# Kernel tuning notes

Hardware: AMD Instinct MI355X
Metric: run time of the kernel (lower is better)

## Reference

```python
import jax, jax.numpy as jnp
import numpy as np

D_K = 1024
D_V = 1024
D_IN = 1024
D_MODEL = 1024
NUM_HEADS = 16


def setup_inputs() -> dict:
    key = jax.random.key(0)
    k1, k2, k3, k4, k5 = jax.random.split(key, 5)
    x = jax.random.normal(k1, (4, 2048, D_IN), dtype=jnp.float32)
    # trunc_normal init approximated by clipped normal
    W_Q = jnp.clip(jax.random.normal(k2, (D_K, D_IN), dtype=jnp.float32), -2.0, 2.0)
    W_K = jnp.clip(jax.random.normal(k3, (D_K, D_IN), dtype=jnp.float32), -2.0, 2.0)
    W_V = jnp.clip(jax.random.normal(k4, (D_V, D_IN), dtype=jnp.float32), -2.0, 2.0)
    W_O = jnp.clip(jax.random.normal(k5, (D_MODEL, D_V), dtype=jnp.float32), -2.0, 2.0)
    return {"x": x, "W_Q": W_Q, "W_K": W_K, "W_V": W_V, "W_O": W_O}


def reference(x, W_Q, W_K, W_V, W_O):
    b, s, _ = x.shape
    h = NUM_HEADS
    hd_k = D_K // h
    hd_v = D_V // h
    wq = W_Q.reshape(h, hd_k, D_IN)
    wk = W_K.reshape(h, hd_k, D_IN)
    wv = W_V.reshape(h, hd_v, D_IN)
    # project: [b, h, s, head_dim]
    q = jnp.einsum('hkd,bsd->bhsk', wq, x)
    k = jnp.einsum('hkd,bsd->bhsk', wk, x)
    v = jnp.einsum('hvd,bsd->bhsv', wv, x)
    scale = 1.0 / jnp.sqrt(jnp.float32(hd_k))
    scores = jnp.einsum('bhnk,bhmk->bhnm', q, k) * scale  # [b,h,s,s]
    causal = jnp.tril(jnp.ones((s, s), dtype=bool))
    scores = jnp.where(causal, scores, -jnp.inf)
    attn = jax.nn.softmax(scores, axis=-1)
    out = jnp.einsum('bhnm,bhmv->bhnv', attn, v)  # [b,h,s,hd_v]
    out = out.transpose(0, 2, 1, 3).reshape(b, s, D_V)  # concat heads
    return jnp.einsum('ov,bsv->bso', W_O, out)
```

## Files before the change

### kernel.cpp

```cpp
#include <hip/hip_runtime.h>
#include <hip/hip_bf16.h>

typedef __bf16 bf16_t;
typedef __bf16 bf16x4 __attribute__((ext_vector_type(4)));
typedef __bf16 bf16x8 __attribute__((ext_vector_type(8)));
typedef float f32x4 __attribute__((ext_vector_type(4)));

#define MFMA16(a, b, c) __builtin_amdgcn_mfma_f32_16x16x32_bf16((a), (b), (c), 0, 0, 0)

#if __has_builtin(__builtin_amdgcn_exp2f)
#define EXP2(x) __builtin_amdgcn_exp2f(x)
#else
#define EXP2(x) exp2f(x)
#endif

__device__ inline void g2l16(const void* g, void* l) {
    __builtin_amdgcn_global_load_lds((const __attribute__((address_space(1))) void*)g,
                                     (__attribute__((address_space(3))) void*)l, 16, 0, 0);
}

__global__ __launch_bounds__(256) void cvt_split_k(const float* __restrict__ src,
                                                   bf16_t* __restrict__ hi,
                                                   bf16_t* __restrict__ lo, int n4) {
    int i = blockIdx.x * 256 + threadIdx.x;
    if (i < n4) {
        float4 v = reinterpret_cast<const float4*>(src)[i];
        bf16x4 h, l;
        float f;
        f = v.x; h[0] = (__bf16)f; l[0] = (__bf16)(f - (float)h[0]);
        f = v.y; h[1] = (__bf16)f; l[1] = (__bf16)(f - (float)h[1]);
        f = v.z; h[2] = (__bf16)f; l[2] = (__bf16)(f - (float)h[2]);
        f = v.w; h[3] = (__bf16)f; l[3] = (__bf16)(f - (float)h[3]);
        reinterpret_cast<bf16x4*>(hi)[i] = h;
        reinterpret_cast<bf16x4*>(lo)[i] = l;
    }
}

__global__ __launch_bounds__(256) void cvt_weights_k(const float* __restrict__ Wq,
                                                     const float* __restrict__ Wk,
                                                     const float* __restrict__ Wv,
                                                     const float* __restrict__ Wo,
                                                     bf16_t* __restrict__ WQKh, bf16_t* __restrict__ WQKl,
                                                     bf16_t* __restrict__ Wvh, bf16_t* __restrict__ Woh) {
    const int i = blockIdx.x * 256 + threadIdx.x;
    const int which = blockIdx.y;
    if (which <= 1) {
        const float c = (which == 0) ? 0.125f * 1.4426950408889634f : 1.0f;
        const int off = which * 262144;
        float4 v = reinterpret_cast<const float4*>(which == 0 ? Wq : Wk)[i];
        bf16x4 h, l;
        float f;
        f = v.x * c; h[0] = (__bf16)f; l[0] = (__bf16)(f - (float)h[0]);
        f = v.y * c; h[1] = (__bf16)f; l[1] = (__bf16)(f - (float)h[1]);
        f = v.z * c; h[2] = (__bf16)f; l[2] = (__bf16)(f - (float)h[2]);
        f = v.w * c; h[3] = (__bf16)f; l[3] = (__bf16)(f - (float)h[3]);
        reinterpret_cast<bf16x4*>(WQKh)[i + off] = h;
        reinterpret_cast<bf16x4*>(WQKl)[i + off] = l;
    } else {
        float4 v = reinterpret_cast<const float4*>(which == 2 ? Wv : Wo)[i];
        bf16x4 o;
        o[0] = (__bf16)v.x; o[1] = (__bf16)v.y; o[2] = (__bf16)v.z; o[3] = (__bf16)v.w;
        reinterpret_cast<bf16x4*>(which == 2 ? Wvh : Woh)[i] = o;
    }
}

template <int LGX>
__device__ inline void xcd_tile(int& bm, int& bn) {
    const int id = blockIdx.y * (1 << LGX) + blockIdx.x;
    const int cpx = ((1 << LGX) * gridDim.y) >> 3;
    const int swz = (id & 7) * cpx + (id >> 3);
    bn = swz & ((1 << LGX) - 1);
    bm = swz >> LGX;
}

template <int MODE>
__global__ __launch_bounds__(256) void gemm_bt(const bf16_t* __restrict__ A,
                                               const bf16_t* __restrict__ B,
                                               void* __restrict__ Cout,
                                               int M, int N, int K) {
    __shared__ __align__(16) bf16_t As[128 * 32];
    __shared__ __align__(16) bf16_t Bs[128 * 32];
    const int tid = threadIdx.x;
    const int w = tid >> 6, lane = tid & 63;
    const int l15 = lane & 15, g = lane >> 4;
    const int wr = w >> 1, wc = w & 1;
    int bm, bn;
    xcd_tile<3>(bm, bn);

    const f32x4 fz = {0.f, 0.f, 0.f, 0.f};
    f32x4 acc[4][4];
#pragma unroll
    for (int m = 0; m < 4; m++)
#pragma unroll
        for (int n = 0; n < 4; n++) acc[m][n] = fz;

    const bf16_t* Ab = A + (size_t)bm * 128 * K;
    const bf16_t* Bb = B + (size_t)bn * 128 * K;
    const int rowL = w * 16 + (lane >> 2);
    const int c8 = (lane & 3) * 8;
    char* AsD = (char*)As + w * 1024;
    char* BsD = (char*)Bs + w * 1024;

    for (int k0 = 0; k0 < K; k0 += 32) {
        g2l16(Ab + (size_t)rowL * K + k0 + c8, AsD);
        g2l16(Ab + (size_t)(rowL + 64) * K + k0 + c8, AsD + 4096);
        g2l16(Bb + (size_t)rowL * K + k0 + c8, BsD);
        g2l16(Bb + (size_t)(rowL + 64) * K + k0 + c8, BsD + 4096);
        __syncthreads();

        bf16x8 af[4], bfr[4];
        const bf16x8* Ap = reinterpret_cast<const bf16x8*>(As + (wr * 64 + l15) * 32 + g * 8);
#pragma unroll
        for (int m = 0; m < 4; m++) af[m] = Ap[m * 64];
        const bf16x8* Bp = reinterpret_cast<const bf16x8*>(Bs + (wc * 64 + l15) * 32 + g * 8);
#pragma unroll
        for (int n = 0; n < 4; n++) bfr[n] = Bp[n * 64];
#pragma unroll
        for (int m = 0; m < 4; m++)
#pragma unroll
            for (int n = 0; n < 4; n++) acc[m][n] = MFMA16(af[m], bfr[n], acc[m][n]);
        __syncthreads();
    }

    const int row0 = bm * 128 + wr * 64 + g * 4;
    const int col0 = bn * 128 + wc * 64 + l15;
#pragma unroll
    for (int m = 0; m < 4; m++)
#pragma unroll
        for (int n = 0; n < 4; n++)
#pragma unroll
            for (int r = 0; r < 4; r++) {
                int row = row0 + m * 16 + r;
                int col = col0 + n * 16;
                float v = acc[m][n][r];
                if (MODE == 0) {
                    ((bf16_t*)Cout)[(size_t)row * N + col] = (__bf16)v;
                } else if (MODE == 1) {
                    int b = row >> 11, s = row & 2047;
                    ((bf16_t*)Cout)[((size_t)b * N + col) * 2048 + s] = (__bf16)v;
                } else {
                    ((float*)Cout)[(size_t)row * N + col] = v;
                }
            }
}

__global__ __launch_bounds__(256) void gemm_splitQK(const bf16_t* __restrict__ Ah,
                                                    const bf16_t* __restrict__ Al,
                                                    const bf16_t* __restrict__ Bh,
                                                    const bf16_t* __restrict__ Bl,
                                                    bf16_t* __restrict__ Qh,
                                                    bf16_t* __restrict__ Ql,
                                                    bf16_t* __restrict__ Kh,
                                                    bf16_t* __restrict__ Kl,
                                                    int K) {
    __shared__ __align__(16) bf16_t Ash[128 * 32];
    __shared__ __align__(16) bf16_t Asl[128 * 32];
    __shared__ __align__(16) bf16_t Bsh[128 * 32];
    __shared__ __align__(16) bf16_t Bsl[128 * 32];
    const int tid = threadIdx.x;
    const int w = tid >> 6, lane = tid & 63;
    const int l15 = lane & 15, g = lane >> 4;
    const int wr = w >> 1, wc = w & 1;
    int bm, bn;
    xcd_tile<4>(bm, bn);

    const f32x4 fz = {0.f, 0.f, 0.f, 0.f};
    f32x4 acc[4][4];
#pragma unroll
    for (int m = 0; m < 4; m++)
#pragma unroll
        for (int n = 0; n < 4; n++) acc[m][n] = fz;

    const size_t aoff = (size_t)bm * 128 * K;
    const size_t boff = (size_t)bn * 128 * K;
    const int rowL = w * 16 + (lane >> 2);
    const int c8 = (lane & 3) * 8;
    const size_t g0 = (size_t)rowL * K + c8;
    const size_t g1 = (size_t)(rowL + 64) * K + c8;

    for (int k0 = 0; k0 < K; k0 += 32) {
        g2l16(Ah + aoff + g0 + k0, (char*)Ash + w * 1024);
        g2l16(Ah + aoff + g1 + k0, (char*)Ash + w * 1024 + 4096);
        g2l16(Al + aoff + g0 + k0, (char*)Asl + w * 1024);
        g2l16(Al + aoff + g1 + k0, (char*)Asl + w * 1024 + 4096);
        g2l16(Bh + boff + g0 + k0, (char*)Bsh + w * 1024);
        g2l16(Bh + boff + g1 + k0, (char*)Bsh + w * 1024 + 4096);
        g2l16(Bl + boff + g0 + k0, (char*)Bsl + w * 1024);
        g2l16(Bl + boff + g1 + k0, (char*)Bsl + w * 1024 + 4096);
        __syncthreads();

        bf16x8 ah[4], al[4], bh[4], bl[4];
        const int ao = (wr * 64 + l15) * 32 + g * 8;
        const int bo = (wc * 64 + l15) * 32 + g * 8;
#pragma unroll
        for (int m = 0; m < 4; m++) {
            ah[m] = *reinterpret_cast<const bf16x8*>(Ash + ao + m * 512);
            al[m] = *reinterpret_cast<const bf16x8*>(Asl + ao + m * 512);
        }
#pragma unroll
        for (int n = 0; n < 4; n++) {
            bh[n] = *reinterpret_cast<const bf16x8*>(Bsh + bo + n * 512);
            bl[n] = *reinterpret_cast<const bf16x8*>(Bsl + bo + n * 512);
        }
#pragma unroll
        for (int m = 0; m < 4; m++)
#pragma unroll
            for (int n = 0; n < 4; n++) {
                acc[m][n] = MFMA16(ah[m], bh[n], acc[m][n]);
                acc[m][n] = MFMA16(al[m], bh[n], acc[m][n]);
                acc[m][n] = MFMA16(ah[m], bl[n], acc[m][n]);
            }
        __syncthreads();
    }

    bf16_t* Ch = (bn < 8) ? Qh : Kh;
    bf16_t* Cl = (bn < 8) ? Ql : Kl;
    const int row0 = bm * 128 + wr * 64 + g * 4;
    const int col0 = (bn * 128 + wc * 64 + l15) & 1023;
#pragma unroll
    for (int m = 0; m < 4; m++)
#pragma unroll
        for (int n = 0; n < 4; n++)
#pragma unroll
            for (int r = 0; r < 4; r++) {
                size_t idx = (size_t)(row0 + m * 16 + r) * 1024 + col0 + n * 16;
                float v = acc[m][n][r];
                bf16_t h = (__bf16)v;
                Ch[idx] = h;
                Cl[idx] = (__bf16)(v - (float)h);
            }
}

__global__ __launch_bounds__(256) void attn_k(const bf16_t* __restrict__ Qh,
                                              const bf16_t* __restrict__ Ql,
                                              const bf16_t* __restrict__ Kh,
                                              const bf16_t* __restrict__ Kl,
                                              const bf16_t* __restrict__ Vt,
                                              bf16_t* __restrict__ Opart,
                                              float* __restrict__ ML) {
    const int px = blockIdx.x;
    const int h = blockIdx.y;
    const int b = blockIdx.z >> 1, hf = blockIdx.z & 1;
    const int tid = threadIdx.x, w = tid >> 6, lane = tid & 63;
    const int l15 = lane & 15, g = lane >> 4;

    __shared__ __align__(16) bf16_t Ks[4096];
    __shared__ __align__(16) bf16_t Ls[4096];
    __shared__ __align__(16) bf16_t Vs[4096];
    __shared__ __align__(16) bf16_t Ps[4][1024];

    const size_t boff = (size_t)b * 2048 * 1024;
    const size_t vbase = (size_t)b * 1024 * 2048 + (size_t)(h * 64) * 2048;

    const int sr = tid >> 3;
    const int sc = tid & 7;
    const int wo0 = sr * 8 + (sc ^ (sr & 7));
    const int wo1 = wo0 + 256;

    int4 sK0, sK1, sL0, sL1, sV0, sV1;
#define STAGE_LOAD(T)                                                               \
    do {                                                                            \
        const int kv0_ = (T) * 64;                                                  \
        const bf16_t* kp = Kh + boff + (size_t)(kv0_ + sr) * 1024 + h * 64 + sc * 8;\
        const bf16_t* lp = Kl + boff + (size_t)(kv0_ + sr) * 1024 + h * 64 + sc * 8;\
        const bf16_t* vp = Vt + vbase + (size_t)sr * 2048 + kv0_ + sc * 8;          \
        sK0 = *(const int4*)kp; sK1 = *(const int4*)(kp + 32 * 1024);               \
        sL0 = *(const int4*)lp; sL1 = *(const int4*)(lp + 32 * 1024);               \
        sV0 = *(const int4*)vp; sV1 = *(const int4*)(vp + 32 * 2048);               \
    } while (0)
#define STAGE_WRITE()                                                               \
    do {                                                                            \
        ((int4*)Ks)[wo0] = sK0; ((int4*)Ks)[wo1] = sK1;                             \
        ((int4*)Ls)[wo0] = sL0; ((int4*)Ls)[wo1] = sL1;                             \
        ((int4*)Vs)[wo0] = sV0; ((int4*)Vs)[wo1] = sV1;                             \
    } while (0)

    const f32x4 fz = {0.f, 0.f, 0.f, 0.f};
    bf16_t* Op = Opart + (size_t)hf * 8 * 1024 * 1024;
    float* MLp = ML + (size_t)hf * 8192 * 16 * 2;

#pragma unroll 1
    for (int it = 0; it < 2; ++it) {
        const int qt = it ? (15 - px) : px;
        const int qrw = qt * 128 + w * 32;

        bf16x8 qhf[2][2], qlf[2][2];
#pragma unroll
        for (int m = 0; m < 2; m++)
#pragma unroll
            for (int kk = 0; kk < 2; kk++) {
                size_t qi = boff + (size_t)(qrw + m * 16 + l15) * 1024 + h * 64 + kk * 32 + g * 8;
                qhf[m][kk] = *reinterpret_cast<const bf16x8*>(Qh + qi);
                qlf[m][kk] = *reinterpret_cast<const bf16x8*>(Ql + qi);
            }

        f32x4 oacc[2][4];
#pragma unroll
        for (int m = 0; m < 2; m++)
#pragma unroll
            for (int n = 0; n < 4; n++) oacc[m][n] = fz;
        float mst[2] = {-__builtin_inff(), -__builtin_inff()};
        float lst[2] = {0.f, 0.f};

        const int t0 = hf ? qt + 1 : 0;
        const int t1 = hf ? 2 * qt + 1 : qt;
        STAGE_LOAD(t0);
        STAGE_WRITE();
        __syncthreads();

        for (int t = t0; t <= t1; ++t) {
            const int kv0 = t * 64;
            if (t < t1) STAGE_LOAD(t + 1);

            if (kv0 <= qrw + 31) {
                f32x4 st[2][4];
#pragma unroll
                for (int m = 0; m < 2; m++)
#pragma unroll
                    for (int n = 0; n < 4; n++) st[m][n] = fz;
                __builtin_amdgcn_s_setprio(1);
#pragma unroll
                for (int kk = 0; kk < 2; kk++)
#pragma unroll
                    for (int n = 0; n < 4; n++) {
                        const int off = (n * 16 + l15) * 64 + (((kk * 4 + g) ^ (l15 & 7)) << 3);
                        bf16x8 khf = *reinterpret_cast<const bf16x8*>(&Ks[off]);
                        bf16x8 klf = *reinterpret_cast<const bf16x8*>(&Ls[off]);
#pragma unroll
                        for (int m = 0; m < 2; m++) {
                            st[m][n] = MFMA16(khf, qhf[m][kk], st[m][n]);
                            st[m][n] = MFMA16(khf, qlf[m][kk], st[m][n]);
                            st[m][n] = MFMA16(klf, qhf[m][kk], st[m][n]);
                        }
                    }
                __builtin_amdgcn_s_setprio(0);

                const bool diag = (kv0 + 63 > qrw);
#pragma unroll
                for (int m = 0; m < 2; m++) {
                    const int qrow = qrw + m * 16 + l15;
                    float pmax = -__builtin_inff();
                    if (diag) {
                        const int klim = qrow - kv0;
#pragma unroll
                        for (int n = 0; n < 4; n++)
#pragma unroll
                            for (int r = 0; r < 4; r++) {
                                float s = st[m][n][r];
                                if (n * 16 + g * 4 + r > klim) s = -__builtin_inff();
                                st[m][n][r] = s;
                                pmax = fmaxf(pmax, s);
                            }
                    } else {
#pragma unroll
                        for (int n = 0; n < 4; n++)
#pragma unroll
                            for (int r = 0; r < 4; r++) pmax = fmaxf(pmax, st[m][n][r]);
                    }
                    pmax = fmaxf(pmax, __shfl_xor(pmax, 16));
                    pmax = fmaxf(pmax, __shfl_xor(pmax, 32));
                    const float mn = fmaxf(mst[m], pmax);
                    const float alpha = EXP2(mst[m] - mn);
                    mst[m] = mn;
                    float rs = 0.f;
#pragma unroll
                    for (int n = 0; n < 4; n++)
#pragma unroll
                        for (int r = 0; r < 4; r++) {
                            float pe = EXP2(st[m][n][r] - mn);
                            st[m][n][r] = pe;
                            rs += pe;
                        }
                    rs += __shfl_xor(rs, 16);
                    rs += __shfl_xor(rs, 32);
                    lst[m] = lst[m] * alpha + rs;
#pragma unroll
                    for (int n = 0; n < 4; n++) oacc[m][n] *= alpha;

#pragma unroll
                    for (int n = 0; n < 4; n++) {
                        bf16x4 p4;
#pragma unroll
                        for (int r = 0; r < 4; r++) p4[r] = (__bf16)st[m][n][r];
                        const int chunk = (2 * n + (g >> 1)) ^ (l15 & 7);
                        *reinterpret_cast<bf16x4*>(&Ps[w][l15 * 64 + chunk * 8 + (g & 1) * 4]) = p4;
                    }

                    asm volatile("s_waitcnt lgkmcnt(0)" ::: "memory");
                    __builtin_amdgcn_sched_barrier(0);

                    __builtin_amdgcn_s_setprio(1);
#pragma unroll
                    for (int kk = 0; kk < 2; kk++) {
                        bf16x8 pa = *reinterpret_cast<const bf16x8*>(
                            &Ps[w][l15 * 64 + (((kk * 4 + g) ^ (l15 & 7)) << 3)]);
#pragma unroll
                        for (int n = 0; n < 4; n++) {
                            const int voff = (n * 16 + l15) * 64 + (((kk * 4 + g) ^ (l15 & 7)) << 3);
                            bf16x8 vf = *reinterpret_cast<const bf16x8*>(&Vs[voff]);
                            oacc[m][n] = MFMA16(vf, pa, oacc[m][n]);
                        }
                    }
                    __builtin_amdgcn_s_setprio(0);
                }
            }
            __syncthreads();
            if (t < t1) STAGE_WRITE();
            __syncthreads();
        }

#pragma unroll
        for (int m = 0; m < 2; m++) {
            const int qrow = qrw + m * 16 + l15;
#pragma unroll
            for (int n = 0; n < 4; n++) {
                bf16x4 o4;
#pragma unroll
                for (int r = 0; r < 4; r++) o4[r] = (__bf16)oacc[m][n][r];
                *reinterpret_cast<bf16x4*>(&Op[boff + (size_t)qrow * 1024 + h * 64 + n * 16 + g * 4]) = o4;
            }
            if (g == 0) {
                const int grow = b * 2048 + qrow;
                MLp[(grow * 16 + h) * 2 + 0] = mst[m];
                MLp[(grow * 16 + h) * 2 + 1] = lst[m];
            }
        }
    }
#undef STAGE_LOAD
#undef STAGE_WRITE
}

__global__ __launch_bounds__(256) void attn_combine_k(const bf16_t* __restrict__ Op0,
                                                      const bf16_t* __restrict__ Op1,
                                                      const float* __restrict__ ML,
                                                      bf16_t* __restrict__ O) {
    const int t = blockIdx.x * 256 + threadIdx.x;
    const int row = t >> 7;
    const int h = (t >> 3) & 15;
    const float m1 = ML[(row * 16 + h) * 2 + 0];
    const float l1 = ML[(row * 16 + h) * 2 + 1];
    const float m2 = ML[(8192 * 16 + row * 16 + h) * 2 + 0];
    const float l2 = ML[(8192 * 16 + row * 16 + h) * 2 + 1];
    const float mx = fmaxf(m1, m2);
    float w1 = (l1 > 0.f) ? EXP2(m1 - mx) : 0.f;
    float w2 = (l2 > 0.f) ? EXP2(m2 - mx) : 0.f;
    const float inv = 1.f / (l1 * w1 + l2 * w2);
    w1 *= inv; w2 *= inv;
    bf16x8 a = reinterpret_cast<const bf16x8*>(Op0)[t];
    bf16x8 c = reinterpret_cast<const bf16x8*>(Op1)[t];
    bf16x8 o;
#pragma unroll
    for (int i = 0; i < 8; i++) o[i] = (__bf16)((float)a[i] * w1 + (float)c[i] * w2);
    reinterpret_cast<bf16x8*>(O)[t] = o;
}

extern "C" void kernel_launch(void* const* d_in, const int* in_sizes, int n_in,
                              void* d_out, int out_size, void* d_ws, size_t ws_size,
                              hipStream_t stream) {
    const float* x  = (const float*)d_in[0];
    const float* Wq = (const float*)d_in[1];
    const float* Wk = (const float*)d_in[2];
    const float* Wv = (const float*)d_in[3];
    const float* Wo = (const float*)d_in[4];

    char* ws = (char*)d_ws;
    const size_t MB = (size_t)1 << 20;
    bf16_t* xh   = (bf16_t*)(ws);
    bf16_t* xl   = (bf16_t*)(ws + 16 * MB);
    bf16_t* Qh   = (bf16_t*)(ws + 32 * MB);
    bf16_t* Ql   = (bf16_t*)(ws + 48 * MB);
    bf16_t* Kh   = (bf16_t*)(ws + 64 * MB);
    bf16_t* Kl   = (bf16_t*)(ws + 80 * MB);
    bf16_t* Vt   = (bf16_t*)(ws + 96 * MB);
    bf16_t* Ob   = (bf16_t*)(ws + 112 * MB);
    bf16_t* WQKh = (bf16_t*)(ws + 128 * MB);
    bf16_t* WQKl = (bf16_t*)(ws + 132 * MB);
    bf16_t* Wvh  = (bf16_t*)(ws + 136 * MB);
    bf16_t* Woh  = (bf16_t*)(ws + 138 * MB);
    bf16_t* Opart = (bf16_t*)(ws);
    float*  ML    = (float*)(ws + 128 * MB);

    cvt_split_k<<<8192, 256, 0, stream>>>(x, xh, xl, 2097152);
    cvt_weights_k<<<dim3(1024, 4), 256, 0, stream>>>(Wq, Wk, Wv, Wo,
                                                     WQKh, WQKl, Wvh, Woh);

    gemm_splitQK<<<dim3(16, 64), 256, 0, stream>>>(xh, xl, WQKh, WQKl,
                                                   Qh, Ql, Kh, Kl, 1024);
    gemm_bt<1><<<dim3(8, 64), 256, 0, stream>>>(xh, Wvh, Vt, 8192, 1024, 1024);

    attn_k<<<dim3(8, 16, 8), 256, 0, stream>>>(Qh, Ql, Kh, Kl, Vt, Opart, ML);
    attn_combine_k<<<4096, 256, 0, stream>>>(Opart, Opart + (size_t)8 * 1024 * 1024, ML, Ob);

    gemm_bt<2><<<dim3(8, 64), 256, 0, stream>>>(Ob, Woh, d_out, 8192, 1024, 1024);
}
```

Measured before the change: 296.5 us.

## Stage V-transpose epilogue in LDS, remap attention blocks, lazily rescale softmax

The MODE 1 GEMM epilogue now transposes the tile through a padded LDS buffer and writes V^T with 16-byte stores instead of scattered 2-byte strided stores. The attention kernel remaps its block index so that neighbouring blocks share heads, batches and K/V data, aiming for better cache locality. Online softmax now skips the running-max update and output rescale unless some lane's max grew by more than 8 (log2 units), which saves exps and multiplies. The lazy rescale lets probabilities run up to 2^8 before bf16 rounding, a small precision risk, and the extra LDS tile raises shared-memory use in the GEMM.

Result: slower. 355.7 us (+20.0%).

```diff
diff --git a/kernel.cpp b/kernel.cpp
--- a/kernel.cpp
+++ b/kernel.cpp
@@ -122,26 +122,52 @@
         __syncthreads();
     }
 
-    const int row0 = bm * 128 + wr * 64 + g * 4;
-    const int col0 = bn * 128 + wc * 64 + l15;
-#pragma unroll
-    for (int m = 0; m < 4; m++)
-#pragma unroll
-        for (int n = 0; n < 4; n++)
-#pragma unroll
-            for (int r = 0; r < 4; r++) {
-                int row = row0 + m * 16 + r;
-                int col = col0 + n * 16;
-                float v = acc[m][n][r];
-                if (MODE == 0) {
-                    ((bf16_t*)Cout)[(size_t)row * N + col] = (__bf16)v;
-                } else if (MODE == 1) {
-                    int b = row >> 11, s = row & 2047;
-                    ((bf16_t*)Cout)[((size_t)b * N + col) * 2048 + s] = (__bf16)v;
-                } else {
-                    ((float*)Cout)[(size_t)row * N + col] = v;
+    if constexpr (MODE == 1) {
+        __shared__ __align__(16) bf16_t Ct[128][130];
+        const int colL = wc * 64 + l15;
+        const int rowB = wr * 64 + g * 4;
+#pragma unroll
+        for (int m = 0; m < 4; m++)
+#pragma unroll
+            for (int n = 0; n < 4; n++) {
+                bf16x4 c4;
+#pragma unroll
+                for (int r = 0; r < 4; r++) c4[r] = (__bf16)acc[m][n][r];
+                *reinterpret_cast<bf16x4*>(&Ct[colL + n * 16][rowB + m * 16]) = c4;
+            }
+        __syncthreads();
+        const int bb = (bm * 128) >> 11;
+        const int s0 = (bm * 128) & 2047;
+        const int vg = tid >> 3, scc = tid & 7;
+        bf16_t* Vtb = (bf16_t*)Cout + (size_t)bb * 1024 * 2048;
+#pragma unroll
+        for (int u = 0; u < 4; u++)
+#pragma unroll
+            for (int hh = 0; hh < 2; hh++) {
+                const int v = u * 32 + vg;
+                const int s = hh * 64 + scc * 8;
+                *reinterpret_cast<int4*>(&Vtb[(size_t)(bn * 128 + v) * 2048 + s0 + s]) =
+                    *reinterpret_cast<const int4*>(&Ct[v][s]);
+            }
+    } else {
+        const int row0 = bm * 128 + wr * 64 + g * 4;
+        const int col0 = bn * 128 + wc * 64 + l15;
+#pragma unroll
+        for (int m = 0; m < 4; m++)
+#pragma unroll
+            for (int n = 0; n < 4; n++)
+#pragma unroll
+                for (int r = 0; r < 4; r++) {
+                    int row = row0 + m * 16 + r;
+                    int col = col0 + n * 16;
+                    float v = acc[m][n][r];
+                    if (MODE == 0) {
+                        ((bf16_t*)Cout)[(size_t)row * N + col] = (__bf16)v;
+                    } else {
+                        ((float*)Cout)[(size_t)row * N + col] = v;
+                    }
                 }
-            }
+    }
 }
 
 __global__ __launch_bounds__(256) void gemm_splitQK(const bf16_t* __restrict__ Ah,
@@ -238,9 +264,12 @@
                                               const bf16_t* __restrict__ Vt,
                                               bf16_t* __restrict__ Opart,
                                               float* __restrict__ ML) {
-    const int px = blockIdx.x;
-    const int h = blockIdx.y;
-    const int b = blockIdx.z >> 1, hf = blockIdx.z & 1;
+    const int L = (int)blockIdx.x + 8 * ((int)blockIdx.y + 16 * (int)blockIdx.z);
+    const int px = (L >> 3) & 7;
+    const int G = (L & 7) + ((L >> 6) << 3);
+    const int h = G & 15;
+    const int zz = G >> 4;
+    const int b = zz >> 1, hf = zz & 1;
     const int tid = threadIdx.x, w = tid >> 6, lane = tid & 63;
     const int l15 = lane & 15, g = lane >> 4;
 
@@ -359,23 +388,26 @@
                     }
                     pmax = fmaxf(pmax, __shfl_xor(pmax, 16));
                     pmax = fmaxf(pmax, __shfl_xor(pmax, 32));
-                    const float mn = fmaxf(mst[m], pmax);
-                    const float alpha = EXP2(mst[m] - mn);
-                    mst[m] = mn;
+                    if (!__all(pmax - mst[m] <= 8.f)) {
+                        const float mn = fmaxf(mst[m], pmax);
+                        const float alpha = EXP2(mst[m] - mn);
+                        mst[m] = mn;
+                        lst[m] *= alpha;
+#pragma unroll
+                        for (int n = 0; n < 4; n++) oacc[m][n] *= alpha;
+                    }
                     float rs = 0.f;
 #pragma unroll
                     for (int n = 0; n < 4; n++)
 #pragma unroll
                         for (int r = 0; r < 4; r++) {
-                            float pe = EXP2(st[m][n][r] - mn);
+                            float pe = EXP2(st[m][n][r] - mst[m]);
                             st[m][n][r] = pe;
                             rs += pe;
                         }
                     rs += __shfl_xor(rs, 16);
                     rs += __shfl_xor(rs, 32);
-                    lst[m] = lst[m] * alpha + rs;
-#pragma unroll
-                    for (int n = 0; n < 4; n++) oacc[m][n] *= alpha;
+                    lst[m] += rs;
 
 #pragma unroll
                     for (int n = 0; n < 4; n++) {
```
